# Performance work log

Measured on AMD Instinct MI355X. Metric: run time of the kernel, lower is better.

## Reference

```python
import jax, jax.numpy as jnp
import numpy as np

DIM = 768
N_HEADS = 12
HEAD_DIM = DIM // N_HEADS
SCALE = HEAD_DIM ** -0.5


def setup_inputs() -> dict:
    key = jax.random.key(0)
    ks = jax.random.split(key, 5)
    B, T = 8, 1024
    x = jax.random.normal(ks[0], (B, T, DIM), dtype=jnp.float32)
    # nn.Linear(dim, 3*dim): weight shape [3*dim, dim], bias [3*dim]
    qkv_w = jax.random.normal(ks[1], (3 * DIM, DIM), dtype=jnp.float32) * (DIM ** -0.5)
    qkv_b = jax.random.normal(ks[2], (3 * DIM,), dtype=jnp.float32) * 0.02
    proj_w = jax.random.normal(ks[3], (DIM, DIM), dtype=jnp.float32) * (DIM ** -0.5)
    proj_b = jax.random.normal(ks[4], (DIM,), dtype=jnp.float32) * 0.02
    return {"x": x, "qkv_w": qkv_w, "qkv_b": qkv_b, "proj_w": proj_w, "proj_b": proj_b}


def reference(x, qkv_w, qkv_b, proj_w, proj_b):
    B, T, D = x.shape
    # QKV projection: [B,T,3D]
    qkv = x @ qkv_w.T + qkv_b
    qkv = qkv.reshape(B, T, 3, N_HEADS, HEAD_DIM)
    qkv = jnp.transpose(qkv, (2, 0, 3, 1, 4))  # [3,B,H,T,hd]
    q, k, v = qkv[0], qkv[1], qkv[2]
    # scores [B,H,T,T]
    scores = jnp.einsum('bhqd,bhkd->bhqk', q, k) * SCALE
    attn = jax.nn.softmax(scores, axis=-1)
    out = jnp.einsum('bhqk,bhkd->bhqd', attn, v)  # [B,H,T,hd]
    out = jnp.transpose(out, (0, 2, 1, 3)).reshape(B, T, D)
    out = out @ proj_w.T + proj_b
    return out
```

## Files before the change

### kernel.cpp

```cpp
#include <hip/hip_runtime.h>

#define DEVINL __device__ __forceinline__

typedef float f32x4 __attribute__((ext_vector_type(4)));
typedef short s16x8 __attribute__((ext_vector_type(8)));
typedef short s16x4 __attribute__((ext_vector_type(4)));

DEVINL short f2bf(float f) {
  union { float f; unsigned u; } x; x.f = f;
  unsigned r = x.u + 0x7fffu + ((x.u >> 16) & 1u);
  return (short)(r >> 16);
}

#if defined(__has_builtin)
#if __has_builtin(__builtin_amdgcn_mfma_f32_16x16x16bf16_1k)
#define HAVE_MFMA16 1
#endif
#endif

DEVINL f32x4 mfma16(s16x4 a, s16x4 b, f32x4 c) {
#ifdef HAVE_MFMA16
  return __builtin_amdgcn_mfma_f32_16x16x16bf16_1k(a, b, c, 0, 0, 0);
#else
  f32x4 d;
  asm volatile("v_mfma_f32_16x16x16_bf16 %0, %1, %2, %3\n\ts_nop 7"
               : "=v"(d) : "v"(a), "v"(b), "v"(c));
  return d;
#endif
}

#define MFMA32(a, b, c) __builtin_amdgcn_mfma_f32_16x16x32_bf16((a), (b), (c), 0, 0, 0)

#define AS1(p) ((const __attribute__((address_space(1))) void*)(p))
#define AS3(p) ((__attribute__((address_space(3))) void*)(p))

__global__ __launch_bounds__(256) void cast3(const float* __restrict__ a,
                                             const float* __restrict__ b,
                                             const float* __restrict__ c,
                                             short* __restrict__ o) {
  const int NA = 8192 * 768, NB2 = 2304 * 768, NC = 768 * 768;
  const int NT = (NA + NB2 + NC) / 4;
  for (int qd = blockIdx.x * 256 + threadIdx.x; qd < NT; qd += gridDim.x * 256) {
    int i = qd * 4;
    const float* src; int off;
    if (i < NA) { src = a; off = i; }
    else if (i < NA + NB2) { src = b; off = i - NA; }
    else { src = c; off = i - NA - NB2; }
    f32x4 v = *(const f32x4*)(src + off);
    s16x4 ov;
    ov[0] = f2bf(v[0]); ov[1] = f2bf(v[1]); ov[2] = f2bf(v[2]); ov[3] = f2bf(v[3]);
    *(s16x4*)(o + i) = ov;
  }
}

template <int EPI>
__global__ __launch_bounds__(256) void gemm_bt(const short* __restrict__ A,
                                               const short* __restrict__ Bw,
                                               const float* __restrict__ bias,
                                               short* __restrict__ o_q, short* __restrict__ o_k,
                                               short* __restrict__ o_v, float* __restrict__ o_f,
                                               int M, int N, int K, int NB) {
  __shared__ short Alds[128 * 32];
  __shared__ short Blds[128 * 32];
  const int t = threadIdx.x;
  const int w = t >> 6, ln = t & 63;
  const int wr = w >> 1, wc = w & 1;
  const int cpx = gridDim.x >> 3;
  const int orig = (blockIdx.x & 7) * cpx + (blockIdx.x >> 3);
  const int mb = orig / NB, nb = orig % NB;
  const int m0 = mb * 128, n0 = nb * 128;
  const int r16 = ln & 15, g = ln >> 4;
  const int arow = ln >> 2;
  const int acol = (ln & 3) * 8;

  f32x4 acc[4][4] = {};

  for (int k0 = 0; k0 < K; k0 += 32) {
    __syncthreads();
#pragma unroll
    for (int i = 0; i < 2; ++i) {
      int row = i * 64 + w * 16 + arow;
      const short* ga = A + (long)(m0 + row) * K + k0 + acol;
      __builtin_amdgcn_global_load_lds(AS1(ga), AS3(&Alds[(i * 4 + w) * 512]), 16, 0, 0);
      const short* gb = Bw + (long)(n0 + row) * K + k0 + acol;
      __builtin_amdgcn_global_load_lds(AS1(gb), AS3(&Blds[(i * 4 + w) * 512]), 16, 0, 0);
    }
    __syncthreads();
    s16x8 af[4], bfr[4];
#pragma unroll
    for (int mi = 0; mi < 4; ++mi)
      af[mi] = *(const s16x8*)&Alds[(wr * 64 + mi * 16 + r16) * 32 + g * 8];
#pragma unroll
    for (int ni = 0; ni < 4; ++ni)
      bfr[ni] = *(const s16x8*)&Blds[(wc * 64 + ni * 16 + r16) * 32 + g * 8];
#pragma unroll
    for (int mi = 0; mi < 4; ++mi)
#pragma unroll
      for (int ni = 0; ni < 4; ++ni)
        acc[mi][ni] = MFMA32(af[mi], bfr[ni], acc[mi][ni]);
  }

  if (EPI == 0) {
#pragma unroll
    for (int mi = 0; mi < 4; ++mi) {
#pragma unroll
      for (int ni = 0; ni < 4; ++ni) {
        int n = n0 + wc * 64 + ni * 16 + r16;
        float bv = bias[n];
        int which = n / 768;
        int nr = n - which * 768;
        int h = nr >> 6, d = nr & 63;
        short* dst = (which == 0) ? o_q : ((which == 1) ? o_k : o_v);
#pragma unroll
        for (int r = 0; r < 4; ++r) {
          int m = m0 + wr * 64 + mi * 16 + g * 4 + r;
          int b = m >> 10, tr = m & 1023;
          long idx = ((long)(b * 12 + h) * 1024 + tr) * 64 + d;
          dst[idx] = f2bf(acc[mi][ni][r] + bv);
        }
      }
    }
  } else {
#pragma unroll
    for (int mi = 0; mi < 4; ++mi) {
#pragma unroll
      for (int ni = 0; ni < 4; ++ni) {
        int n = n0 + wc * 64 + ni * 16 + r16;
        float bv = bias[n];
#pragma unroll
        for (int r = 0; r < 4; ++r) {
          int m = m0 + wr * 64 + mi * 16 + g * 4 + r;
          o_f[(long)m * N + n] = acc[mi][ni][r] + bv;
        }
      }
    }
  }
}

__global__ __launch_bounds__(256) void attn_kernel(const short* __restrict__ qb,
                                                   const short* __restrict__ kb,
                                                   const short* __restrict__ vb,
                                                   short* __restrict__ ao) {
  __shared__ short Qlds[128 * 72];
  __shared__ short Klds[64 * 72];
  __shared__ short Vtlds[64 * 72];
  const int t = threadIdx.x;
  const int w = t >> 6, ln = t & 63;
  const int r16 = ln & 15, g = ln >> 4;
  const int bh = blockIdx.x >> 3;
  const int qblk = blockIdx.x & 7;
  const int b = bh / 12, h = bh % 12;
  const long base = (long)bh * 65536;
  const int q0 = qblk * 128;

#pragma unroll
  for (int it = 0; it < 4; ++it) {
    int slot = it * 256 + t;
    int row = slot >> 3, d0 = (slot & 7) << 3;
    *(s16x8*)&Qlds[row * 72 + d0] = *(const s16x8*)(qb + base + (long)(q0 + row) * 64 + d0);
  }
  __syncthreads();
  s16x8 qf[2][2];
#pragma unroll
  for (int s = 0; s < 2; ++s) {
    int row = s * 64 + w * 16 + r16;
#pragma unroll
    for (int kh = 0; kh < 2; ++kh)
      qf[s][kh] = *(const s16x8*)&Qlds[row * 72 + kh * 32 + g * 8];
  }

  f32x4 accO[2][4] = {};
  float den[2] = {0.f, 0.f};
  const int vjp = t & 31, vd0 = (t >> 5) << 3;

  for (int kt = 0; kt < 16; ++kt) {
    __syncthreads();
    const short* kp = kb + base + (long)kt * 64 * 64;
#pragma unroll
    for (int it = 0; it < 2; ++it) {
      int slot = it * 256 + t;
      int row = slot >> 3, d0 = (slot & 7) << 3;
      *(s16x8*)&Klds[row * 72 + d0] = *(const s16x8*)(kp + row * 64 + d0);
    }
    const short* vp = vb + base + (long)kt * 64 * 64;
    {
      s16x8 va = *(const s16x8*)(vp + (2 * vjp) * 64 + vd0);
      s16x8 vc = *(const s16x8*)(vp + (2 * vjp + 1) * 64 + vd0);
#pragma unroll
      for (int jj = 0; jj < 8; ++jj) {
        unsigned val = (unsigned)(unsigned short)va[jj] | ((unsigned)(unsigned short)vc[jj] << 16);
        *(unsigned*)&Vtlds[(vd0 + jj) * 72 + 2 * vjp] = val;
      }
    }
    __syncthreads();

    f32x4 st[2][4];
#pragma unroll
    for (int mj = 0; mj < 4; ++mj) {
      s16x8 k0f = *(const s16x8*)&Klds[(mj * 16 + r16) * 72 + g * 8];
      s16x8 k1f = *(const s16x8*)&Klds[(mj * 16 + r16) * 72 + 32 + g * 8];
#pragma unroll
      for (int s = 0; s < 2; ++s) {
        f32x4 z = {};
        z = MFMA32(k0f, qf[s][0], z);
        z = MFMA32(k1f, qf[s][1], z);
        st[s][mj] = z;
      }
    }
    s16x4 pt[2][4];
#pragma unroll
    for (int s = 0; s < 2; ++s) {
#pragma unroll
      for (int mj = 0; mj < 4; ++mj) {
#pragma unroll
        for (int r = 0; r < 4; ++r) {
          float p = __expf(st[s][mj][r] * 0.125f);
          den[s] += p;
          pt[s][mj][r] = f2bf(p);
        }
      }
    }
#pragma unroll
    for (int di = 0; di < 4; ++di) {
#pragma unroll
      for (int mj = 0; mj < 4; ++mj) {
        s16x4 vf = *(const s16x4*)&Vtlds[(di * 16 + r16) * 72 + mj * 16 + g * 4];
        accO[0][di] = mfma16(pt[0][mj], vf, accO[0][di]);
        accO[1][di] = mfma16(pt[1][mj], vf, accO[1][di]);
      }
    }
  }

#pragma unroll
  for (int s = 0; s < 2; ++s) {
    float dsum = den[s];
    dsum += __shfl_xor(dsum, 16);
    dsum += __shfl_xor(dsum, 32);
    float inv[4];
#pragma unroll
    for (int r = 0; r < 4; ++r) {
      float dr = __shfl(dsum, g * 4 + r);
      inv[r] = 1.0f / dr;
    }
    const long orow0 = (long)b * 1024 + q0 + s * 64 + w * 16;
#pragma unroll
    for (int di = 0; di < 4; ++di) {
#pragma unroll
      for (int r = 0; r < 4; ++r) {
        long row = orow0 + g * 4 + r;
        ao[row * 768 + h * 64 + di * 16 + r16] = f2bf(accO[s][di][r] * inv[r]);
      }
    }
  }
}

extern "C" void kernel_launch(void* const* d_in, const int* in_sizes, int n_in,
                              void* d_out, int out_size, void* d_ws, size_t ws_size,
                              hipStream_t stream) {
  const float* x      = (const float*)d_in[0];
  const float* qkv_w  = (const float*)d_in[1];
  const float* qkv_b  = (const float*)d_in[2];
  const float* proj_w = (const float*)d_in[3];
  const float* proj_b = (const float*)d_in[4];
  float* out = (float*)d_out;

  const long BT = 8192, D = 768, D3 = 2304;
  short* ws   = (short*)d_ws;
  short* xb   = ws;
  short* wqkv = xb + BT * D;
  short* wprj = wqkv + D3 * D;
  short* q    = wprj + D * D;
  short* k    = q + BT * D;
  short* v    = k + BT * D;
  short* ao   = v + BT * D;

  cast3<<<2048, 256, 0, stream>>>(x, qkv_w, proj_w, ws);
  gemm_bt<0><<<64 * 18, 256, 0, stream>>>(xb, wqkv, qkv_b, q, k, v, nullptr,
                                          8192, 2304, 768, 18);
  attn_kernel<<<96 * 8, 256, 0, stream>>>(q, k, v, ao);
  gemm_bt<1><<<64 * 6, 256, 0, stream>>>(ao, wprj, proj_b, nullptr, nullptr, nullptr, out,
                                         8192, 768, 768, 6);
}
```

Before: 207.4 us.

## Double-buffer GEMM LDS tiles and register-prefetch K/V tiles in attention

```diff
diff --git a/kernel.cpp b/kernel.cpp
--- a/kernel.cpp
+++ b/kernel.cpp
@@ -33,6 +33,9 @@
 
 #define AS1(p) ((const __attribute__((address_space(1))) void*)(p))
 #define AS3(p) ((__attribute__((address_space(3))) void*)(p))
+#define VMCNT(N) asm volatile("s_waitcnt vmcnt(" #N ")" ::: "memory")
+#define LGKM0() asm volatile("s_waitcnt lgkmcnt(0)" ::: "memory")
+#define SCHED0() __builtin_amdgcn_sched_barrier(0)
 
 __global__ __launch_bounds__(256) void cast3(const float* __restrict__ a,
                                              const float* __restrict__ b,
@@ -53,59 +56,81 @@
   }
 }
 
-template <int EPI>
-__global__ __launch_bounds__(256) void gemm_bt(const short* __restrict__ A,
+template <int EPI, int TN>
+__global__ __launch_bounds__(256) void gemm_db(const short* __restrict__ A,
                                                const short* __restrict__ Bw,
                                                const float* __restrict__ bias,
                                                short* __restrict__ o_q, short* __restrict__ o_k,
                                                short* __restrict__ o_v, float* __restrict__ o_f,
                                                int M, int N, int K, int NB) {
-  __shared__ short Alds[128 * 32];
-  __shared__ short Blds[128 * 32];
+  constexpr int NI = TN / 32;
+  __shared__ short Alds[2][128 * 32];
+  __shared__ short Blds[2][TN * 32];
   const int t = threadIdx.x;
   const int w = t >> 6, ln = t & 63;
   const int wr = w >> 1, wc = w & 1;
   const int cpx = gridDim.x >> 3;
   const int orig = (blockIdx.x & 7) * cpx + (blockIdx.x >> 3);
   const int mb = orig / NB, nb = orig % NB;
-  const int m0 = mb * 128, n0 = nb * 128;
+  const int m0 = mb * 128, n0 = nb * TN;
   const int r16 = ln & 15, g = ln >> 4;
   const int arow = ln >> 2;
   const int acol = (ln & 3) * 8;
 
-  f32x4 acc[4][4] = {};
-
-  for (int k0 = 0; k0 < K; k0 += 32) {
-    __syncthreads();
+  auto stage = [&](int k0, int bufi) {
 #pragma unroll
     for (int i = 0; i < 2; ++i) {
       int row = i * 64 + w * 16 + arow;
       const short* ga = A + (long)(m0 + row) * K + k0 + acol;
-      __builtin_amdgcn_global_load_lds(AS1(ga), AS3(&Alds[(i * 4 + w) * 512]), 16, 0, 0);
+      __builtin_amdgcn_global_load_lds(AS1(ga), AS3(&Alds[bufi][(i * 4 + w) * 512]), 16, 0, 0);
+    }
+#pragma unroll
+    for (int i = 0; i < TN / 64; ++i) {
+      int row = i * 64 + w * 16 + arow;
       const short* gb = Bw + (long)(n0 + row) * K + k0 + acol;
-      __builtin_amdgcn_global_load_lds(AS1(gb), AS3(&Blds[(i * 4 + w) * 512]), 16, 0, 0);
-    }
-    __syncthreads();
-    s16x8 af[4], bfr[4];
+      __builtin_amdgcn_global_load_lds(AS1(gb), AS3(&Blds[bufi][(i * 4 + w) * 512]), 16, 0, 0);
+    }
+  };
+
+  f32x4 acc[4][NI] = {};
+  stage(0, 0);
+  const int NT = K / 32;
+  int cur = 0;
+  for (int tt = 0; tt < NT; ++tt) {
+    if (tt + 1 < NT) {
+      stage((tt + 1) * 32, cur ^ 1);
+      if constexpr (TN == 128) { VMCNT(4); } else { VMCNT(3); }
+    } else {
+      VMCNT(0);
+    }
+    SCHED0();
+    __builtin_amdgcn_s_barrier();
+    SCHED0();
+    s16x8 af[4], bfr[NI];
 #pragma unroll
     for (int mi = 0; mi < 4; ++mi)
-      af[mi] = *(const s16x8*)&Alds[(wr * 64 + mi * 16 + r16) * 32 + g * 8];
-#pragma unroll
-    for (int ni = 0; ni < 4; ++ni)
-      bfr[ni] = *(const s16x8*)&Blds[(wc * 64 + ni * 16 + r16) * 32 + g * 8];
+      af[mi] = *(const s16x8*)&Alds[cur][(wr * 64 + mi * 16 + r16) * 32 + g * 8];
+#pragma unroll
+    for (int ni = 0; ni < NI; ++ni)
+      bfr[ni] = *(const s16x8*)&Blds[cur][(wc * (TN / 2) + ni * 16 + r16) * 32 + g * 8];
 #pragma unroll
     for (int mi = 0; mi < 4; ++mi)
 #pragma unroll
-      for (int ni = 0; ni < 4; ++ni)
+      for (int ni = 0; ni < NI; ++ni)
         acc[mi][ni] = MFMA32(af[mi], bfr[ni], acc[mi][ni]);
+    LGKM0();
+    SCHED0();
+    __builtin_amdgcn_s_barrier();
+    SCHED0();
+    cur ^= 1;
   }
 
   if (EPI == 0) {
 #pragma unroll
     for (int mi = 0; mi < 4; ++mi) {
 #pragma unroll
-      for (int ni = 0; ni < 4; ++ni) {
-        int n = n0 + wc * 64 + ni * 16 + r16;
+      for (int ni = 0; ni < NI; ++ni) {
+        int n = n0 + wc * (TN / 2) + ni * 16 + r16;
         float bv = bias[n];
         int which = n / 768;
         int nr = n - which * 768;
@@ -124,8 +149,8 @@
 #pragma unroll
     for (int mi = 0; mi < 4; ++mi) {
 #pragma unroll
-      for (int ni = 0; ni < 4; ++ni) {
-        int n = n0 + wc * 64 + ni * 16 + r16;
+      for (int ni = 0; ni < NI; ++ni) {
+        int n = n0 + wc * (TN / 2) + ni * 16 + r16;
         float bv = bias[n];
 #pragma unroll
         for (int r = 0; r < 4; ++r) {
@@ -152,6 +177,8 @@
   const int b = bh / 12, h = bh % 12;
   const long base = (long)bh * 65536;
   const int q0 = qblk * 128;
+  const int krow0 = t >> 3, kd0 = (t & 7) << 3;
+  const int vjp = t & 31, vd0 = (t >> 5) << 3;
 
 #pragma unroll
   for (int it = 0; it < 4; ++it) {
@@ -159,6 +186,17 @@
     int row = slot >> 3, d0 = (slot & 7) << 3;
     *(s16x8*)&Qlds[row * 72 + d0] = *(const s16x8*)(qb + base + (long)(q0 + row) * 64 + d0);
   }
+
+  s16x8 kr0, kr1, va, vc;
+  {
+    const short* kp = kb + base;
+    kr0 = *(const s16x8*)(kp + krow0 * 64 + kd0);
+    kr1 = *(const s16x8*)(kp + (32 + krow0) * 64 + kd0);
+    const short* vp = vb + base;
+    va = *(const s16x8*)(vp + (2 * vjp) * 64 + vd0);
+    vc = *(const s16x8*)(vp + (2 * vjp + 1) * 64 + vd0);
+  }
+
   __syncthreads();
   s16x8 qf[2][2];
 #pragma unroll
@@ -171,26 +209,23 @@
 
   f32x4 accO[2][4] = {};
   float den[2] = {0.f, 0.f};
-  const int vjp = t & 31, vd0 = (t >> 5) << 3;
 
   for (int kt = 0; kt < 16; ++kt) {
     __syncthreads();
-    const short* kp = kb + base + (long)kt * 64 * 64;
-#pragma unroll
-    for (int it = 0; it < 2; ++it) {
-      int slot = it * 256 + t;
-      int row = slot >> 3, d0 = (slot & 7) << 3;
-      *(s16x8*)&Klds[row * 72 + d0] = *(const s16x8*)(kp + row * 64 + d0);
-    }
-    const short* vp = vb + base + (long)kt * 64 * 64;
-    {
-      s16x8 va = *(const s16x8*)(vp + (2 * vjp) * 64 + vd0);
-      s16x8 vc = *(const s16x8*)(vp + (2 * vjp + 1) * 64 + vd0);
-#pragma unroll
-      for (int jj = 0; jj < 8; ++jj) {
-        unsigned val = (unsigned)(unsigned short)va[jj] | ((unsigned)(unsigned short)vc[jj] << 16);
-        *(unsigned*)&Vtlds[(vd0 + jj) * 72 + 2 * vjp] = val;
-      }
+    *(s16x8*)&Klds[krow0 * 72 + kd0] = kr0;
+    *(s16x8*)&Klds[(32 + krow0) * 72 + kd0] = kr1;
+#pragma unroll
+    for (int jj = 0; jj < 8; ++jj) {
+      unsigned val = (unsigned)(unsigned short)va[jj] | ((unsigned)(unsigned short)vc[jj] << 16);
+      *(unsigned*)&Vtlds[(vd0 + jj) * 72 + 2 * vjp] = val;
+    }
+    if (kt + 1 < 16) {
+      const short* kp = kb + base + (long)(kt + 1) * 4096;
+      kr0 = *(const s16x8*)(kp + krow0 * 64 + kd0);
+      kr1 = *(const s16x8*)(kp + (32 + krow0) * 64 + kd0);
+      const short* vp = vb + base + (long)(kt + 1) * 4096;
+      va = *(const s16x8*)(vp + (2 * vjp) * 64 + vd0);
+      vc = *(const s16x8*)(vp + (2 * vjp + 1) * 64 + vd0);
     }
     __syncthreads();
 
@@ -275,9 +310,9 @@
   short* ao   = v + BT * D;
 
   cast3<<<2048, 256, 0, stream>>>(x, qkv_w, proj_w, ws);
-  gemm_bt<0><<<64 * 18, 256, 0, stream>>>(xb, wqkv, qkv_b, q, k, v, nullptr,
-                                          8192, 2304, 768, 18);
+  gemm_db<0, 128><<<64 * 18, 256, 0, stream>>>(xb, wqkv, qkv_b, q, k, v, nullptr,
+                                               8192, 2304, 768, 18);
   attn_kernel<<<96 * 8, 256, 0, stream>>>(q, k, v, ao);
-  gemm_bt<1><<<64 * 6, 256, 0, stream>>>(ao, wprj, proj_b, nullptr, nullptr, nullptr, out,
-                                         8192, 768, 768, 6);
-}
+  gemm_db<1, 64><<<128 * 6, 256, 0, stream>>>(ao, wprj, proj_b, nullptr, nullptr, nullptr, out,
+                                              8192, 768, 768, 12);
+}
```

New measurement: 199.3 us. -3.9%, faster.
